# Kernel optimization log

Measured on AMD Instinct MI355X. Metric: run time of the kernel, lower is better.

Reference implementation:

```python
import jax, jax.numpy as jnp
import numpy as np

DELTA_V = 0.5
DELTA_D = 1.5
ALPHA = 1.0
BETA = 1.0
GAMMA = 0.001
K = 33  # segment count: id 0 = background, 1..32 = instances (matches fill_max)


def setup_inputs() -> dict:
    key = jax.random.key(0)
    k1, k2 = jax.random.split(key)
    embeddings = jax.random.normal(k1, (8, 16, 512, 512), dtype=jnp.float32)
    instance_masks = jax.random.randint(k2, (8, 512, 512), 0, K, dtype=jnp.int32)
    return {"embeddings": embeddings, "instance_masks": instance_masks}


def _safe_norm(sq):
    # sqrt with zero-safe gradient: returns 0 where sq == 0
    pos = sq > 0
    return jnp.sqrt(jnp.where(pos, sq, 1.0)) * pos.astype(sq.dtype)


def _per_image(emb, mask):
    # emb: (E, H, W), mask: (H, W)
    E = emb.shape[0]
    emb_flat = emb.reshape(E, -1).T            # (N, E)
    ids = mask.reshape(-1)                      # (N,)

    counts = jax.ops.segment_sum(jnp.ones(ids.shape, jnp.float32), ids, num_segments=K)  # (K,)
    sums = jax.ops.segment_sum(emb_flat, ids, num_segments=K)                             # (K, E)
    counts_c = jnp.maximum(counts, 1.0)
    means = sums / counts_c[:, None]            # (K, E)

    present = counts[1:] > 0                    # (K-1,) which instance ids appear
    n_inst = present.sum().astype(jnp.float32)

    # variance (pull) term: per-pixel distance to own instance mean
    diff = emb_flat - means[ids]                # (N, E)
    pix_d = _safe_norm(jnp.sum(diff * diff, axis=1))
    var_term = jnp.maximum(pix_d - DELTA_V, 0.0) ** 2
    var_per = jax.ops.segment_sum(var_term, ids, num_segments=K)[1:]  # drop background seg
    var_loss = jnp.sum(jnp.where(present, var_per / counts_c[1:], 0.0)) / jnp.maximum(n_inst, 1.0)

    # distance (push) term: pairwise centroid distances among present instances
    m = means[1:]                               # (K-1, E)
    dsq = jnp.sum((m[:, None, :] - m[None, :, :]) ** 2, axis=-1)
    dmat = _safe_norm(dsq)
    pair_mask = (jnp.triu(jnp.ones((K - 1, K - 1), bool), 1)
                 & present[:, None] & present[None, :])
    n_pairs = pair_mask.sum().astype(jnp.float32)
    dist_term = jnp.maximum(2.0 * DELTA_D - dmat, 0.0) ** 2
    dist_loss = jnp.sum(jnp.where(pair_mask, dist_term, 0.0)) / jnp.maximum(n_pairs, 1.0)
    dist_loss = dist_loss * (n_inst > 1.0).astype(jnp.float32)

    # regularization: mean centroid norm over present instances
    mean_norms = _safe_norm(jnp.sum(m * m, axis=1))
    reg_loss = jnp.sum(jnp.where(present, mean_norms, 0.0)) / jnp.maximum(n_inst, 1.0)

    valid = (n_inst > 0.0).astype(jnp.float32)
    return var_loss * valid, dist_loss * valid, reg_loss * valid, valid


def reference(embeddings, instance_masks):
    v, d, r, valid = jax.vmap(_per_image)(embeddings, instance_masks)
    vs = jnp.maximum(valid.sum(), 1.0)
    var_loss = v.sum() / vs
    dist_loss = d.sum() / vs
    reg_loss = r.sum() / vs
    total = ALPHA * var_loss + BETA * dist_loss + GAMMA * reg_loss
    return jnp.stack([total, var_loss, dist_loss, reg_loss])
```

## Files before the change

### kernel.cpp

```cpp
#include <hip/hip_runtime.h>
#include <math.h>


#define B 8
#define E 16
#define HW (512*512)
#define BLK 256
#define P1_BPI 128
#define P2_BPI 128
#define P2_VPB (HW / 4 / P2_BPI)

typedef __attribute__((ext_vector_type(8)))  short short8;
typedef __attribute__((ext_vector_type(16))) float floatx16;

__device__ __forceinline__ float atomAddF(float* p, float v) {
  return unsafeAtomicAdd(p, v);
}

__device__ __forceinline__ unsigned pack_bf(float a, float b) {
  return __builtin_amdgcn_perm(__float_as_uint(b), __float_as_uint(a), 0x07060302u);
}

struct Tile { int4 ma, mb_, mc, md; float4 f0, f1; };

__device__ __forceinline__ void load_tile(Tile& T, const int* __restrict__ mb,
                                          const float* __restrict__ pl, int tl, bool ld_emb) {
  const int4* mp = (const int4*)(mb + tl * 16);
  T.ma = mp[0]; T.mb_ = mp[1]; T.mc = mp[2]; T.md = mp[3];
  if (ld_emb) {
    T.f0 = ((const float4*)(pl + tl * 16))[0];
    T.f1 = ((const float4*)(pl + tl * 16))[1];
  }
}

__global__ __launch_bounds__(BLK) void pass1_kernel(
    const float* __restrict__ emb, const int* __restrict__ mask,
    float* __restrict__ gsum ) {
  __shared__ float lred[4][32][33];
  const int b    = blockIdx.y;
  const int t    = threadIdx.x;
  const int lane = t & 63;
  const int wv   = __builtin_amdgcn_readfirstlane(t >> 6);
  const int n    = lane & 31;
  const int h    = lane >> 5;
  const int myid = n + 1;
  const bool ld  = (n < 16);

  const int ppw    = HW / (P1_BPI * 4);
  const int base   = (blockIdx.x * 4 + wv) * ppw;
  const int ntiles = ppw / 16;

  const int*   __restrict__ mb = mask + (size_t)b * HW + base;
  const float* __restrict__ pl = emb + ((size_t)b * E + (n & 15)) * HW + base + 8 * h;

  floatx16 acc;
#pragma unroll
  for (int i = 0; i < 16; ++i) acc[i] = 0.f;

  Tile cur, nxt;
  load_tile(cur, mb, pl, 0, ld);

#pragma unroll 2
  for (int tl = 0; tl < ntiles; ++tl) {
    if (tl + 1 < ntiles) load_tile(nxt, mb, pl, tl + 1, ld);

    short8 bf;
    if (ld) {
      union { uint4 u; short8 s; } cv;
      cv.u.x = pack_bf(cur.f0.x, cur.f0.y);
      cv.u.y = pack_bf(cur.f0.z, cur.f0.w);
      cv.u.z = pack_bf(cur.f1.x, cur.f1.y);
      cv.u.w = pack_bf(cur.f1.z, cur.f1.w);
      bf = cv.s;
    } else if (n == 16) {
      const short one = (short)0x3F80;
      bf[0]=one; bf[1]=one; bf[2]=one; bf[3]=one; bf[4]=one; bf[5]=one; bf[6]=one; bf[7]=one;
    } else {
      bf[0]=0; bf[1]=0; bf[2]=0; bf[3]=0; bf[4]=0; bf[5]=0; bf[6]=0; bf[7]=0;
    }

    const int4 A0 = h ? cur.mc : cur.ma;
    const int4 A1 = h ? cur.md : cur.mb_;
    short8 af;
    af[0] = (A0.x == myid) ? (short)0x3F80 : (short)0;
    af[1] = (A0.y == myid) ? (short)0x3F80 : (short)0;
    af[2] = (A0.z == myid) ? (short)0x3F80 : (short)0;
    af[3] = (A0.w == myid) ? (short)0x3F80 : (short)0;
    af[4] = (A1.x == myid) ? (short)0x3F80 : (short)0;
    af[5] = (A1.y == myid) ? (short)0x3F80 : (short)0;
    af[6] = (A1.z == myid) ? (short)0x3F80 : (short)0;
    af[7] = (A1.w == myid) ? (short)0x3F80 : (short)0;

    acc = __builtin_amdgcn_mfma_f32_32x32x16_bf16(af, bf, acc, 0, 0, 0);
    cur = nxt;
  }

#pragma unroll
  for (int r = 0; r < 16; ++r) {
    const int row = (r & 3) + 8 * (r >> 2) + 4 * h;
    lred[wv][row][n] = acc[r];
  }
  __syncthreads();

  for (int i = t; i < 32 * 32; i += BLK) {
    const int row = i >> 5, col = i & 31;
    if (col < 17) {
      const float s = lred[0][row][col] + lred[1][row][col]
                    + lred[2][row][col] + lred[3][row][col];
      atomAddF(&gsum[((size_t)b * 32 + row) * 17 + col], s);
    }
  }
}

__global__ __launch_bounds__(BLK) void pass2_kernel(
    const float* __restrict__ emb, const int* __restrict__ mask,
    const float* __restrict__ gsum, float* __restrict__ var_per ) {
  __shared__ float mean4[33][4][4];
  __shared__ float lvar[33][8];
  const int b = blockIdx.y;
  const int t = threadIdx.x;
  const int c = t & 7;

  for (int i = t; i < 33 * 16; i += BLK) {
    const int k = i >> 4, e = i & 15;
    float m = 0.f;
    if (k >= 1) {
      const float cnt = gsum[((size_t)b * 32 + (k - 1)) * 17 + 16];
      const float cc  = cnt > 1.f ? cnt : 1.f;
      m = gsum[((size_t)b * 32 + (k - 1)) * 17 + e] / cc;
    }
    const int j = e >> 2;
    mean4[k][(j + k) & 3][e & 3] = m;
  }
  for (int i = t; i < 33 * 8; i += BLK) (&lvar[0][0])[i] = 0.f;
  __syncthreads();

  const int4*  __restrict__ maskv = (const int4*)(mask + (size_t)b * HW);
  const float* __restrict__ embb  = emb + (size_t)b * E * HW;
  const int v0 = blockIdx.x * P2_VPB;

#pragma unroll 1
  for (int v = v0 + t; v < v0 + P2_VPB; v += BLK) {
    const int4 id = maskv[v];
    float4 x[E];
#pragma unroll
    for (int e = 0; e < E; ++e) x[e] = ((const float4*)(embb + (size_t)e * HW))[v];

    float d0 = 0.f, d1 = 0.f, d2 = 0.f, d3 = 0.f;
#pragma unroll
    for (int j = 0; j < 4; ++j) {
      const float4 m0 = *(const float4*)&mean4[id.x][(j + id.x) & 3][0];
      const float4 m1 = *(const float4*)&mean4[id.y][(j + id.y) & 3][0];
      const float4 m2 = *(const float4*)&mean4[id.z][(j + id.z) & 3][0];
      const float4 m3 = *(const float4*)&mean4[id.w][(j + id.w) & 3][0];
      const float4 a0 = x[4 * j + 0], a1 = x[4 * j + 1];
      const float4 a2 = x[4 * j + 2], a3 = x[4 * j + 3];
      float u;
      u = a0.x - m0.x; d0 += u * u;  u = a1.x - m0.y; d0 += u * u;
      u = a2.x - m0.z; d0 += u * u;  u = a3.x - m0.w; d0 += u * u;
      u = a0.y - m1.x; d1 += u * u;  u = a1.y - m1.y; d1 += u * u;
      u = a2.y - m1.z; d1 += u * u;  u = a3.y - m1.w; d1 += u * u;
      u = a0.z - m2.x; d2 += u * u;  u = a1.z - m2.y; d2 += u * u;
      u = a2.z - m2.z; d2 += u * u;  u = a3.z - m2.w; d2 += u * u;
      u = a0.w - m3.x; d3 += u * u;  u = a1.w - m3.y; d3 += u * u;
      u = a2.w - m3.z; d3 += u * u;  u = a3.w - m3.w; d3 += u * u;
    }
    float hh;
    hh = fmaxf(sqrtf(d0) - 0.5f, 0.f); atomAddF(&lvar[id.x][c], hh * hh);
    hh = fmaxf(sqrtf(d1) - 0.5f, 0.f); atomAddF(&lvar[id.y][c], hh * hh);
    hh = fmaxf(sqrtf(d2) - 0.5f, 0.f); atomAddF(&lvar[id.z][c], hh * hh);
    hh = fmaxf(sqrtf(d3) - 0.5f, 0.f); atomAddF(&lvar[id.w][c], hh * hh);
  }
  __syncthreads();

  if (t >= 1 && t < 33) {
    float s = 0.f;
#pragma unroll
    for (int cc = 0; cc < 8; ++cc) s += lvar[t][cc];
    atomAddF(&var_per[b * 32 + (t - 1)], s);
  }
}

__global__ __launch_bounds__(BLK) void final_kernel(
    const float* __restrict__ gsum, const float* __restrict__ var_per,
    float* __restrict__ out) {
  __shared__ float mean[B][32][E];
  __shared__ float cnts[B][32];
  __shared__ float vb[B], rb[B], db[B], pb[B], nb[B];
  const int t = threadIdx.x;

  if (t < B) { vb[t] = 0.f; rb[t] = 0.f; db[t] = 0.f; pb[t] = 0.f; nb[t] = 0.f; }
  {
    const int bb = t >> 5, k = t & 31;
    const float c  = gsum[((size_t)bb * 32 + k) * 17 + 16];
    const float cc = c > 1.f ? c : 1.f;
    cnts[bb][k] = c;
#pragma unroll
    for (int e = 0; e < E; ++e)
      mean[bb][k][e] = gsum[((size_t)bb * 32 + k) * 17 + e] / cc;
  }
  __syncthreads();

  {
    const int bb = t >> 5, k = t & 31;
    const float c = cnts[bb][k];
    if (c > 0.5f) {
      atomAddF(&nb[bb], 1.f);
      atomAddF(&vb[bb], var_per[bb * 32 + k] / c);
      float sq = 0.f;
#pragma unroll
      for (int e = 0; e < E; ++e) { const float m = mean[bb][k][e]; sq += m * m; }
      atomAddF(&rb[bb], sq > 0.f ? sqrtf(sq) : 0.f);
    }
  }
  __syncthreads();

  for (int idx = t; idx < B * 32 * 32; idx += BLK) {
    const int bb = idx >> 10;
    const int p  = idx & 1023;
    const int i  = p >> 5;
    const int j  = p & 31;
    if (i < j && cnts[bb][i] > 0.5f && cnts[bb][j] > 0.5f) {
      atomAddF(&pb[bb], 1.f);
      float sq = 0.f;
#pragma unroll
      for (int e = 0; e < E; ++e) {
        const float d = mean[bb][i][e] - mean[bb][j][e];
        sq += d * d;
      }
      const float dn = sq > 0.f ? sqrtf(sq) : 0.f;
      const float hh = 3.0f - dn;
      if (hh > 0.f) atomAddF(&db[bb], hh * hh);
    }
  }
  __syncthreads();

  if (t == 0) {
    float sv = 0.f, sd = 0.f, sr = 0.f, svalid = 0.f;
    for (int bb = 0; bb < B; ++bb) {
      const float ni  = nb[bb];
      const float nim = ni > 1.f ? ni : 1.f;
      const float var_b = vb[bb] / nim;
      const float reg_b = rb[bb] / nim;
      const float npm   = pb[bb] > 1.f ? pb[bb] : 1.f;
      const float dist_b = (ni > 1.f) ? (db[bb] / npm) : 0.f;
      const float valid  = ni > 0.f ? 1.f : 0.f;
      sv += var_b * valid;
      sd += dist_b * valid;
      sr += reg_b * valid;
      svalid += valid;
    }
    const float vs = svalid > 1.f ? svalid : 1.f;
    const float var = sv / vs, dist = sd / vs, reg = sr / vs;
    out[0] = var + dist + 0.001f * reg;
    out[1] = var;
    out[2] = dist;
    out[3] = reg;
  }
}

extern "C" void kernel_launch(void* const* d_in, const int* in_sizes, int n_in,
                              void* d_out, int out_size, void* d_ws, size_t ws_size,
                              hipStream_t stream) {
  const float* emb  = (const float*)d_in[0];
  const int*   mask = (const int*)d_in[1];
  float* out = (float*)d_out;

  float* gsum    = (float*)d_ws;
  float* var_per = (float*)((char*)d_ws + (size_t)B * 32 * 17 * 4);

  hipMemsetAsync(d_ws, 0, (size_t)(B * 32 * 17 + B * 32) * 4, stream);

  pass1_kernel<<<dim3(P1_BPI, B), BLK, 0, stream>>>(emb, mask, gsum);
  pass2_kernel<<<dim3(P2_BPI, B), BLK, 0, stream>>>(emb, mask, gsum, var_per);
  final_kernel<<<1, BLK, 0, stream>>>(gsum, var_per, out);
}
```

Measured before the change: 251.7 us.

## Stage masks in LDS, deepen prefetch in pass1, fold per-instance weights in pass2

Pass1 now loads each wave's mask chunk into shared memory once and deepens the embedding prefetch to four tiles in flight. This replaces the single-tile double buffer, so more global loads overlap the MFMA work. Pass2 precomputes 1/count per instance and accumulates the weighted hinge loss in a register, then does a wave-shuffle reduction and one atomic per block. That replaces the per-pixel shared-memory atomics into per-instance bins. The final kernel reads the per-image sum directly. The cost is extra LDS and register use in pass1, plus a changed mean-swizzle pattern in pass2.

```diff
diff --git a/kernel.cpp b/kernel.cpp
--- a/kernel.cpp
+++ b/kernel.cpp
@@ -21,22 +21,11 @@
   return __builtin_amdgcn_perm(__float_as_uint(b), __float_as_uint(a), 0x07060302u);
 }
 
-struct Tile { int4 ma, mb_, mc, md; float4 f0, f1; };
-
-__device__ __forceinline__ void load_tile(Tile& T, const int* __restrict__ mb,
-                                          const float* __restrict__ pl, int tl, bool ld_emb) {
-  const int4* mp = (const int4*)(mb + tl * 16);
-  T.ma = mp[0]; T.mb_ = mp[1]; T.mc = mp[2]; T.md = mp[3];
-  if (ld_emb) {
-    T.f0 = ((const float4*)(pl + tl * 16))[0];
-    T.f1 = ((const float4*)(pl + tl * 16))[1];
-  }
-}
-
 __global__ __launch_bounds__(BLK) void pass1_kernel(
     const float* __restrict__ emb, const int* __restrict__ mask,
     float* __restrict__ gsum ) {
-  __shared__ float lred[4][32][33];
+  __shared__ int4 mstage[4][128];
+  __shared__ __align__(16) float lred[4][32][33];
   const int b    = blockIdx.y;
   const int t    = threadIdx.x;
   const int lane = t & 63;
@@ -47,52 +36,72 @@
   const bool ld  = (n < 16);
 
   const int ppw    = HW / (P1_BPI * 4);
+  const int ntiles = ppw / 16;
   const int base   = (blockIdx.x * 4 + wv) * ppw;
-  const int ntiles = ppw / 16;
-
-  const int*   __restrict__ mb = mask + (size_t)b * HW + base;
+
+  {
+    const int4* __restrict__ mg = (const int4*)(mask + (size_t)b * HW + base);
+    mstage[wv][lane]      = mg[lane];
+    mstage[wv][64 + lane] = mg[64 + lane];
+  }
+  __syncthreads();
+
   const float* __restrict__ pl = emb + ((size_t)b * E + (n & 15)) * HW + base + 8 * h;
 
   floatx16 acc;
 #pragma unroll
   for (int i = 0; i < 16; ++i) acc[i] = 0.f;
 
-  Tile cur, nxt;
-  load_tile(cur, mb, pl, 0, ld);
-
-#pragma unroll 2
-  for (int tl = 0; tl < ntiles; ++tl) {
-    if (tl + 1 < ntiles) load_tile(nxt, mb, pl, tl + 1, ld);
-
-    short8 bf;
+  float4 fb[4][2];
+#pragma unroll
+  for (int u = 0; u < 4; ++u) {
     if (ld) {
-      union { uint4 u; short8 s; } cv;
-      cv.u.x = pack_bf(cur.f0.x, cur.f0.y);
-      cv.u.y = pack_bf(cur.f0.z, cur.f0.w);
-      cv.u.z = pack_bf(cur.f1.x, cur.f1.y);
-      cv.u.w = pack_bf(cur.f1.z, cur.f1.w);
-      bf = cv.s;
-    } else if (n == 16) {
-      const short one = (short)0x3F80;
-      bf[0]=one; bf[1]=one; bf[2]=one; bf[3]=one; bf[4]=one; bf[5]=one; bf[6]=one; bf[7]=one;
-    } else {
-      bf[0]=0; bf[1]=0; bf[2]=0; bf[3]=0; bf[4]=0; bf[5]=0; bf[6]=0; bf[7]=0;
-    }
-
-    const int4 A0 = h ? cur.mc : cur.ma;
-    const int4 A1 = h ? cur.md : cur.mb_;
-    short8 af;
-    af[0] = (A0.x == myid) ? (short)0x3F80 : (short)0;
-    af[1] = (A0.y == myid) ? (short)0x3F80 : (short)0;
-    af[2] = (A0.z == myid) ? (short)0x3F80 : (short)0;
-    af[3] = (A0.w == myid) ? (short)0x3F80 : (short)0;
-    af[4] = (A1.x == myid) ? (short)0x3F80 : (short)0;
-    af[5] = (A1.y == myid) ? (short)0x3F80 : (short)0;
-    af[6] = (A1.z == myid) ? (short)0x3F80 : (short)0;
-    af[7] = (A1.w == myid) ? (short)0x3F80 : (short)0;
-
-    acc = __builtin_amdgcn_mfma_f32_32x32x16_bf16(af, bf, acc, 0, 0, 0);
-    cur = nxt;
+      fb[u][0] = ((const float4*)(pl + u * 16))[0];
+      fb[u][1] = ((const float4*)(pl + u * 16))[1];
+    }
+  }
+
+  for (int tl4 = 0; tl4 < ntiles; tl4 += 4) {
+#pragma unroll
+    for (int u = 0; u < 4; ++u) {
+      const int tl = tl4 + u;
+
+      const int4 A0 = mstage[wv][tl * 4 + 2 * h];
+      const int4 A1 = mstage[wv][tl * 4 + 2 * h + 1];
+
+      short8 af;
+      af[0] = (A0.x == myid) ? (short)0x3F80 : (short)0;
+      af[1] = (A0.y == myid) ? (short)0x3F80 : (short)0;
+      af[2] = (A0.z == myid) ? (short)0x3F80 : (short)0;
+      af[3] = (A0.w == myid) ? (short)0x3F80 : (short)0;
+      af[4] = (A1.x == myid) ? (short)0x3F80 : (short)0;
+      af[5] = (A1.y == myid) ? (short)0x3F80 : (short)0;
+      af[6] = (A1.z == myid) ? (short)0x3F80 : (short)0;
+      af[7] = (A1.w == myid) ? (short)0x3F80 : (short)0;
+
+      short8 bf;
+      if (ld) {
+        union { uint4 u4; short8 s; } cv;
+        cv.u4.x = pack_bf(fb[u][0].x, fb[u][0].y);
+        cv.u4.y = pack_bf(fb[u][0].z, fb[u][0].w);
+        cv.u4.z = pack_bf(fb[u][1].x, fb[u][1].y);
+        cv.u4.w = pack_bf(fb[u][1].z, fb[u][1].w);
+        bf = cv.s;
+      } else if (n == 16) {
+        const short one = (short)0x3F80;
+        bf[0]=one; bf[1]=one; bf[2]=one; bf[3]=one; bf[4]=one; bf[5]=one; bf[6]=one; bf[7]=one;
+      } else {
+        bf[0]=0; bf[1]=0; bf[2]=0; bf[3]=0; bf[4]=0; bf[5]=0; bf[6]=0; bf[7]=0;
+      }
+
+      acc = __builtin_amdgcn_mfma_f32_32x32x16_bf16(af, bf, acc, 0, 0, 0);
+
+      const int tn = tl + 4;
+      if (tn < ntiles && ld) {
+        fb[u][0] = ((const float4*)(pl + tn * 16))[0];
+        fb[u][1] = ((const float4*)(pl + tn * 16))[1];
+      }
+    }
   }
 
 #pragma unroll
@@ -114,12 +123,12 @@
 
 __global__ __launch_bounds__(BLK) void pass2_kernel(
     const float* __restrict__ emb, const int* __restrict__ mask,
-    const float* __restrict__ gsum, float* __restrict__ var_per ) {
-  __shared__ float mean4[33][4][4];
-  __shared__ float lvar[33][8];
+    const float* __restrict__ gsum, float* __restrict__ vsum ) {
+  __shared__ __align__(16) float mean4[33][4][4];
+  __shared__ float winv[33];
+  __shared__ float wred[4];
   const int b = blockIdx.y;
   const int t = threadIdx.x;
-  const int c = t & 7;
 
   for (int i = t; i < 33 * 16; i += BLK) {
     const int k = i >> 4, e = i & 15;
@@ -130,14 +139,22 @@
       m = gsum[((size_t)b * 32 + (k - 1)) * 17 + e] / cc;
     }
     const int j = e >> 2;
-    mean4[k][(j + k) & 3][e & 3] = m;
-  }
-  for (int i = t; i < 33 * 8; i += BLK) (&lvar[0][0])[i] = 0.f;
+    mean4[k][(j + k + (k >> 2)) & 3][e & 3] = m;
+  }
+  if (t < 33) {
+    float w = 0.f;
+    if (t >= 1) {
+      const float cnt = gsum[((size_t)b * 32 + (t - 1)) * 17 + 16];
+      w = cnt > 0.5f ? 1.f / cnt : 0.f;
+    }
+    winv[t] = w;
+  }
   __syncthreads();
 
   const int4*  __restrict__ maskv = (const int4*)(mask + (size_t)b * HW);
   const float* __restrict__ embb  = emb + (size_t)b * E * HW;
   const int v0 = blockIdx.x * P2_VPB;
+  float vacc = 0.f;
 
 #pragma unroll 1
   for (int v = v0 + t; v < v0 + P2_VPB; v += BLK) {
@@ -146,13 +163,18 @@
 #pragma unroll
     for (int e = 0; e < E; ++e) x[e] = ((const float4*)(embb + (size_t)e * HW))[v];
 
+    const int sx = id.x + (id.x >> 2);
+    const int sy = id.y + (id.y >> 2);
+    const int sz = id.z + (id.z >> 2);
+    const int sw = id.w + (id.w >> 2);
+
     float d0 = 0.f, d1 = 0.f, d2 = 0.f, d3 = 0.f;
 #pragma unroll
     for (int j = 0; j < 4; ++j) {
-      const float4 m0 = *(const float4*)&mean4[id.x][(j + id.x) & 3][0];
-      const float4 m1 = *(const float4*)&mean4[id.y][(j + id.y) & 3][0];
-      const float4 m2 = *(const float4*)&mean4[id.z][(j + id.z) & 3][0];
-      const float4 m3 = *(const float4*)&mean4[id.w][(j + id.w) & 3][0];
+      const float4 m0 = *(const float4*)&mean4[id.x][(j + sx) & 3][0];
+      const float4 m1 = *(const float4*)&mean4[id.y][(j + sy) & 3][0];
+      const float4 m2 = *(const float4*)&mean4[id.z][(j + sz) & 3][0];
+      const float4 m3 = *(const float4*)&mean4[id.w][(j + sw) & 3][0];
       const float4 a0 = x[4 * j + 0], a1 = x[4 * j + 1];
       const float4 a2 = x[4 * j + 2], a3 = x[4 * j + 3];
       float u;
@@ -166,30 +188,28 @@
       u = a2.w - m3.z; d3 += u * u;  u = a3.w - m3.w; d3 += u * u;
     }
     float hh;
-    hh = fmaxf(sqrtf(d0) - 0.5f, 0.f); atomAddF(&lvar[id.x][c], hh * hh);
-    hh = fmaxf(sqrtf(d1) - 0.5f, 0.f); atomAddF(&lvar[id.y][c], hh * hh);
-    hh = fmaxf(sqrtf(d2) - 0.5f, 0.f); atomAddF(&lvar[id.z][c], hh * hh);
-    hh = fmaxf(sqrtf(d3) - 0.5f, 0.f); atomAddF(&lvar[id.w][c], hh * hh);
-  }
-  __syncthreads();
-
-  if (t >= 1 && t < 33) {
-    float s = 0.f;
-#pragma unroll
-    for (int cc = 0; cc < 8; ++cc) s += lvar[t][cc];
-    atomAddF(&var_per[b * 32 + (t - 1)], s);
-  }
+    hh = fmaxf(sqrtf(d0) - 0.5f, 0.f); vacc += hh * hh * winv[id.x];
+    hh = fmaxf(sqrtf(d1) - 0.5f, 0.f); vacc += hh * hh * winv[id.y];
+    hh = fmaxf(sqrtf(d2) - 0.5f, 0.f); vacc += hh * hh * winv[id.z];
+    hh = fmaxf(sqrtf(d3) - 0.5f, 0.f); vacc += hh * hh * winv[id.w];
+  }
+
+#pragma unroll
+  for (int off = 32; off >= 1; off >>= 1) vacc += __shfl_down(vacc, off, 64);
+  if ((t & 63) == 0) wred[t >> 6] = vacc;
+  __syncthreads();
+  if (t == 0) atomAddF(&vsum[b], wred[0] + wred[1] + wred[2] + wred[3]);
 }
 
 __global__ __launch_bounds__(BLK) void final_kernel(
-    const float* __restrict__ gsum, const float* __restrict__ var_per,
+    const float* __restrict__ gsum, const float* __restrict__ vsum,
     float* __restrict__ out) {
   __shared__ float mean[B][32][E];
   __shared__ float cnts[B][32];
-  __shared__ float vb[B], rb[B], db[B], pb[B], nb[B];
+  __shared__ float rb[B], db[B], pb[B], nb[B];
   const int t = threadIdx.x;
 
-  if (t < B) { vb[t] = 0.f; rb[t] = 0.f; db[t] = 0.f; pb[t] = 0.f; nb[t] = 0.f; }
+  if (t < B) { rb[t] = 0.f; db[t] = 0.f; pb[t] = 0.f; nb[t] = 0.f; }
   {
     const int bb = t >> 5, k = t & 31;
     const float c  = gsum[((size_t)bb * 32 + k) * 17 + 16];
@@ -206,7 +226,6 @@
     const float c = cnts[bb][k];
     if (c > 0.5f) {
       atomAddF(&nb[bb], 1.f);
-      atomAddF(&vb[bb], var_per[bb * 32 + k] / c);
       float sq = 0.f;
 #pragma unroll
       for (int e = 0; e < E; ++e) { const float m = mean[bb][k][e]; sq += m * m; }
@@ -240,7 +259,7 @@
     for (int bb = 0; bb < B; ++bb) {
       const float ni  = nb[bb];
       const float nim = ni > 1.f ? ni : 1.f;
-      const float var_b = vb[bb] / nim;
+      const float var_b = vsum[bb] / nim;
       const float reg_b = rb[bb] / nim;
       const float npm   = pb[bb] > 1.f ? pb[bb] : 1.f;
       const float dist_b = (ni > 1.f) ? (db[bb] / npm) : 0.f;
@@ -266,12 +285,12 @@
   const int*   mask = (const int*)d_in[1];
   float* out = (float*)d_out;
 
-  float* gsum    = (float*)d_ws;
-  float* var_per = (float*)((char*)d_ws + (size_t)B * 32 * 17 * 4);
-
-  hipMemsetAsync(d_ws, 0, (size_t)(B * 32 * 17 + B * 32) * 4, stream);
+  float* gsum = (float*)d_ws;
+  float* vsum = (float*)((char*)d_ws + (size_t)B * 32 * 17 * 4);
+
+  hipMemsetAsync(d_ws, 0, (size_t)(B * 32 * 17 + B) * 4, stream);
 
   pass1_kernel<<<dim3(P1_BPI, B), BLK, 0, stream>>>(emb, mask, gsum);
-  pass2_kernel<<<dim3(P2_BPI, B), BLK, 0, stream>>>(emb, mask, gsum, var_per);
-  final_kernel<<<1, BLK, 0, stream>>>(gsum, var_per, out);
-}
+  pass2_kernel<<<dim3(P2_BPI, B), BLK, 0, stream>>>(emb, mask, gsum, vsum);
+  final_kernel<<<1, BLK, 0, stream>>>(gsum, vsum, out);
+}
```

Measured after the change: 250.4 us. No clear change (-0.5%).
